# Kernel optimization log

Hardware: AMD Instinct MI355X
Metric: run time of the kernel (lower is better)

## Reference

```python
import jax, jax.numpy as jnp
import numpy as np

N = 20000   # nodes (ROIs, scaled up)
F = 20      # node_feat_dim
D = 256     # hidden_dim
H = 8       # heads
DK = D // H # 32
L = 3       # layers
S = 4       # sleep stages
E = 320000  # edges per stage


def _ln(x, g, b):
    mu = x.mean(-1, keepdims=True)
    v = ((x - mu) ** 2).mean(-1, keepdims=True)
    return (x - mu) / jnp.sqrt(v + 1e-5) * g + b


def setup_inputs() -> dict:
    key = jax.random.key(0)
    ks = jax.random.split(key, 16)
    rn = lambda k, s, sc=0.02: jax.random.normal(k, s, jnp.float32) * sc
    return {
        "x": jax.random.normal(ks[0], (N, F), jnp.float32),
        "edge_index": jax.random.randint(ks[1], (S, 2, E), 0, N, jnp.int32),
        "sc_mask": jax.random.randint(ks[2], (S, E), 0, 2, jnp.int32),
        "fc_weights": jax.random.normal(ks[3], (S, E), jnp.float32),
        "in_w": rn(ks[4], (F, D)), "in_b": jnp.zeros((D,), jnp.float32),
        "stage_emb": rn(ks[5], (S, D)),
        "Wq": rn(ks[6], (L, D, D)), "Wk": rn(ks[7], (L, D, D)),
        "Wv": rn(ks[8], (L, D, D)),
        "Wo": rn(ks[9], (L, D, D)), "bo": jnp.zeros((L, D), jnp.float32),
        "ln1_g": jnp.ones((L, D), jnp.float32), "ln1_b": jnp.zeros((L, D), jnp.float32),
        "ln2_g": jnp.ones((L, D), jnp.float32), "ln2_b": jnp.zeros((L, D), jnp.float32),
        "ffn_w1": rn(ks[10], (L, D, 4 * D)), "ffn_b1": jnp.zeros((L, 4 * D), jnp.float32),
        "ffn_w2": rn(ks[11], (L, 4 * D, D)), "ffn_b2": jnp.zeros((L, D), jnp.float32),
        "lam": jnp.full((L,), 0.5, jnp.float32),
        "fus_w": rn(ks[12], (S * D, D)), "fus_b": jnp.zeros((D,), jnp.float32),
        "out_g": jnp.ones((D,), jnp.float32), "out_b": jnp.zeros((D,), jnp.float32),
    }


def reference(x, edge_index, sc_mask, fc_weights, in_w, in_b, stage_emb,
              Wq, Wk, Wv, Wo, bo, ln1_g, ln1_b, ln2_g, ln2_b,
              ffn_w1, ffn_b1, ffn_w2, ffn_b2, lam, fus_w, fus_b, out_g, out_b):
    scale = DK ** 0.5
    stage_outs = []
    for k in range(S):  # fixed small stage count
        src, dst = edge_index[k, 0], edge_index[k, 1]
        sc = sc_mask[k].astype(jnp.float32)
        fcw = fc_weights[k]
        h = x @ in_w + in_b + stage_emb[k]
        for l in range(L):  # fixed small layer count
            Q = (h @ Wq[l]).reshape(N, H, DK)
            K = (h @ Wk[l]).reshape(N, H, DK)
            V = (h @ Wv[l]).reshape(N, H, DK)
            # edge-wise gathered dot-product scores  [E, H]
            attn = (Q[dst] * K[src]).sum(-1) / scale
            attn = attn * sc[:, None] + lam[l] * fcw[:, None]
            # segment softmax grouped by destination node (PyG softmax)
            m = jax.ops.segment_max(attn, dst, num_segments=N)
            e = jnp.exp(attn - m[dst])
            s = jax.ops.segment_sum(e, dst, num_segments=N)
            a = e / (s[dst] + 1e-16)
            # scatter-add weighted V_j  [N, H, DK]
            agg = jax.ops.segment_sum(a[:, :, None] * V[src], dst, num_segments=N)
            out = agg.reshape(N, D) @ Wo[l] + bo[l]
            out = _ln(out + h, ln1_g[l], ln1_b[l])  # residual_proj is Identity (in==out)
            f = jax.nn.gelu(out @ ffn_w1[l] + ffn_b1[l], approximate=False)
            f = f @ ffn_w2[l] + ffn_b2[l]
            h = _ln(out + f, ln2_g[l], ln2_b[l])
        stage_outs.append(h)
    h_concat = jnp.concatenate(stage_outs, axis=-1)  # [N, S*D]
    return _ln(h_concat @ fus_w + fus_b, out_g, out_b)
```

## Files before the change

kernel.cpp:

```cpp
#include <hip/hip_runtime.h>
#include <hip/hip_bf16.h>
#include <math.h>

#define N_NODES 20000
#define FDIM 20
#define DDIM 256
#define HH 8
#define LL 3
#define SS 4
#define EE 320000

typedef __attribute__((ext_vector_type(8))) short bf16x8;
typedef __attribute__((ext_vector_type(8))) unsigned short u16x8;
typedef __attribute__((ext_vector_type(4))) float f32x4;

__device__ inline unsigned short f2bf(float f) {
  unsigned u = __float_as_uint(f);
  unsigned r = u + 0x7FFFu + ((u >> 16) & 1u);
  return (unsigned short)(r >> 16);
}
__device__ inline float bf2f(unsigned short u) {
  return __uint_as_float(((unsigned)u) << 16);
}

__global__ __launch_bounds__(256) void gemm_f32_kernel(
    const float* __restrict__ A, const float* __restrict__ B,
    const float* __restrict__ bias, float* __restrict__ C,
    int M, int Nc, int K)
{
  __shared__ float As[16][65];
  __shared__ float Bs[16][65];
  const int tid = threadIdx.x;
  const int tx = tid & 15, ty = tid >> 4;
  const int row0 = blockIdx.y * 64, col0 = blockIdx.x * 64;
  const int am = tid >> 2, ak = (tid & 3) * 4;
  const int bk = tid >> 4, bc = (tid & 15) * 4;
  float acc[4][4] = {};
  for (int k0 = 0; k0 < K; k0 += 16) {
    float4 av = make_float4(0.f, 0.f, 0.f, 0.f);
    int garow = row0 + am;
    if (garow < M) {
      if (k0 + ak + 3 < K) {
        av = *(const float4*)(A + (size_t)garow * K + k0 + ak);
      } else {
        float t[4];
        #pragma unroll
        for (int j = 0; j < 4; j++)
          t[j] = (k0 + ak + j < K) ? A[(size_t)garow * K + k0 + ak + j] : 0.f;
        av = make_float4(t[0], t[1], t[2], t[3]);
      }
    }
    As[ak + 0][am] = av.x; As[ak + 1][am] = av.y;
    As[ak + 2][am] = av.z; As[ak + 3][am] = av.w;
    float4 bv = make_float4(0.f, 0.f, 0.f, 0.f);
    if (k0 + bk < K)
      bv = *(const float4*)(B + (size_t)(k0 + bk) * Nc + col0 + bc);
    Bs[bk][bc + 0] = bv.x; Bs[bk][bc + 1] = bv.y;
    Bs[bk][bc + 2] = bv.z; Bs[bk][bc + 3] = bv.w;
    __syncthreads();
    #pragma unroll
    for (int kk = 0; kk < 16; kk++) {
      float a[4], b[4];
      #pragma unroll
      for (int i = 0; i < 4; i++) a[i] = As[kk][ty * 4 + i];
      #pragma unroll
      for (int j = 0; j < 4; j++) b[j] = Bs[kk][tx * 4 + j];
      #pragma unroll
      for (int i = 0; i < 4; i++)
        #pragma unroll
        for (int j = 0; j < 4; j++)
          acc[i][j] = fmaf(a[i], b[j], acc[i][j]);
    }
    __syncthreads();
  }
  #pragma unroll
  for (int i = 0; i < 4; i++) {
    int row = row0 + ty * 4 + i;
    if (row >= M) continue;
    int col = col0 + tx * 4;
    float4 v;
    float* vp = &v.x;
    #pragma unroll
    for (int j = 0; j < 4; j++) vp[j] = acc[i][j] + bias[col + j];
    *(float4*)(C + (size_t)row * Nc + col) = v;
  }
}

template<int ACT>
__global__ __launch_bounds__(256) void mfma_gemm64(
    const unsigned short* __restrict__ A, const unsigned short* __restrict__ BT,
    const float* __restrict__ bias, unsigned short* __restrict__ Cb,
    int ldc, int M, int K, int ldb)
{
  __shared__ unsigned short As[2][64][40];
  __shared__ unsigned short Bs[2][128][40];
  const int tid = threadIdx.x, lane = tid & 63, wid = tid >> 6;
  const int wr = (wid >> 1) * 32, wc = (wid & 1) * 64;
  const int row0 = blockIdx.y * 64, col0 = blockIdx.x * 128;
  const int sr = tid >> 2, sc = (tid & 3) * 8;
  const int c15 = lane & 15, g16 = lane >> 4;
  const int KT = K >> 5;
  f32x4 acc[2][4] = {};
  int garow = row0 + sr; if (garow > M - 1) garow = M - 1;
  const unsigned short* Aptr = A + (size_t)garow * K + sc;
  const unsigned short* Bptr0 = BT + (size_t)(col0 + sr) * ldb + sc;
  const unsigned short* Bptr1 = BT + (size_t)(col0 + 64 + sr) * ldb + sc;
  u16x8 aA, b0A, b1A, aB, b0B, b1B;

#define LD64(ra, rb0, rb1, k0) { ra = *(const u16x8*)(Aptr + (k0)); \
  rb0 = *(const u16x8*)(Bptr0 + (k0)); rb1 = *(const u16x8*)(Bptr1 + (k0)); }
#define WR64(buf, ra, rb0, rb1) { *(u16x8*)&As[buf][sr][sc] = ra; \
  *(u16x8*)&Bs[buf][sr][sc] = rb0; *(u16x8*)&Bs[buf][64 + sr][sc] = rb1; }
#define MM64(buf) { bf16x8 af[2], bfv[4]; \
  _Pragma("unroll") for (int mi = 0; mi < 2; mi++) \
    af[mi] = *(const bf16x8*)&As[buf][wr + mi * 16 + c15][g16 * 8]; \
  _Pragma("unroll") for (int ni = 0; ni < 4; ni++) \
    bfv[ni] = *(const bf16x8*)&Bs[buf][wc + ni * 16 + c15][g16 * 8]; \
  _Pragma("unroll") for (int mi = 0; mi < 2; mi++) \
  _Pragma("unroll") for (int ni = 0; ni < 4; ni++) \
    acc[mi][ni] = __builtin_amdgcn_mfma_f32_16x16x32_bf16(af[mi], bfv[ni], acc[mi][ni], 0, 0, 0); }

  LD64(aA, b0A, b1A, 0);
  WR64(0, aA, b0A, b1A);
  if (KT > 1) LD64(aA, b0A, b1A, 32);
  __syncthreads();
  for (int kt = 0; kt < KT; kt += 2) {
    if (kt + 2 < KT) LD64(aB, b0B, b1B, (kt + 2) * 32);
    MM64(0);
    if (kt + 1 < KT) WR64(1, aA, b0A, b1A);
    __syncthreads();
    if (kt + 1 >= KT) break;
    if (kt + 3 < KT) LD64(aA, b0A, b1A, (kt + 3) * 32);
    MM64(1);
    if (kt + 2 < KT) WR64(0, aB, b0B, b1B);
    __syncthreads();
  }
#undef LD64
#undef WR64
#undef MM64
  #pragma unroll
  for (int mi = 0; mi < 2; mi++) {
    #pragma unroll
    for (int ni = 0; ni < 4; ni++) {
      int col = col0 + wc + ni * 16 + c15;
      float bval = bias ? bias[col] : 0.f;
      #pragma unroll
      for (int j = 0; j < 4; j++) {
        int row = row0 + wr + mi * 16 + g16 * 4 + j;
        if (row < M) {
          float t = acc[mi][ni][j] + bval;
          if (ACT == 1) t = 0.5f * t * (1.f + erff(t * 0.7071067811865475f));
          Cb[(size_t)row * ldc + col] = f2bf(t);
        }
      }
    }
  }
}

template<int KTILES, int DO_LN, int ACCUM>
__global__ __launch_bounds__(256) void gemm_ln_kernel(
    const unsigned short* __restrict__ A, const unsigned short* __restrict__ BT,
    const float* __restrict__ bias, const float* __restrict__ resid,
    const float* __restrict__ gv, const float* __restrict__ bv,
    float* __restrict__ outf, unsigned short* __restrict__ outb,
    int M, int ldb, int bk0)
{
  constexpr int K = KTILES * 32;
  __shared__ unsigned short As[2][32][40];
  __shared__ unsigned short Bs[2][256][40];
  __shared__ float red[32][4][2];
  __shared__ float stats[32][2];
  const int tid = threadIdx.x, lane = tid & 63, w = tid >> 6;
  const int row0 = blockIdx.x * 32;
  const int sr2 = tid >> 3, sc2 = (tid & 7) * 4;
  const int sr = tid >> 2, sc = (tid & 3) * 8;
  const int g16 = lane >> 4, c15 = lane & 15;
  f32x4 acc[2][4] = {};
  int garow = row0 + sr2; if (garow > M - 1) garow = M - 1;
  const unsigned short* Aptr = A + (size_t)garow * K + sc2;
  const unsigned short* Bptr0 = BT + (size_t)(0 * 64 + sr) * ldb + bk0 + sc;
  const unsigned short* Bptr1 = BT + (size_t)(1 * 64 + sr) * ldb + bk0 + sc;
  const unsigned short* Bptr2 = BT + (size_t)(2 * 64 + sr) * ldb + bk0 + sc;
  const unsigned short* Bptr3 = BT + (size_t)(3 * 64 + sr) * ldb + bk0 + sc;
  ushort4 aA, aB;
  u16x8 bA0, bA1, bA2, bA3, bB0, bB1, bB2, bB3;

#define LDGL(ra, r0, r1, r2, r3, k0) { ra = *(const ushort4*)(Aptr + (k0)); \
  r0 = *(const u16x8*)(Bptr0 + (k0)); r1 = *(const u16x8*)(Bptr1 + (k0)); \
  r2 = *(const u16x8*)(Bptr2 + (k0)); r3 = *(const u16x8*)(Bptr3 + (k0)); }
#define WRGL(buf, ra, r0, r1, r2, r3) { *(ushort4*)&As[buf][sr2][sc2] = ra; \
  *(u16x8*)&Bs[buf][0 * 64 + sr][sc] = r0; *(u16x8*)&Bs[buf][1 * 64 + sr][sc] = r1; \
  *(u16x8*)&Bs[buf][2 * 64 + sr][sc] = r2; *(u16x8*)&Bs[buf][3 * 64 + sr][sc] = r3; }
#define MMGL(buf) { bf16x8 af[2], bfv[4]; \
  _Pragma("unroll") for (int mi = 0; mi < 2; mi++) \
    af[mi] = *(const bf16x8*)&As[buf][mi * 16 + c15][g16 * 8]; \
  _Pragma("unroll") for (int ni = 0; ni < 4; ni++) \
    bfv[ni] = *(const bf16x8*)&Bs[buf][w * 64 + ni * 16 + c15][g16 * 8]; \
  _Pragma("unroll") for (int mi = 0; mi < 2; mi++) \
  _Pragma("unroll") for (int ni = 0; ni < 4; ni++) \
    acc[mi][ni] = __builtin_amdgcn_mfma_f32_16x16x32_bf16(af[mi], bfv[ni], acc[mi][ni], 0, 0, 0); }

  LDGL(aA, bA0, bA1, bA2, bA3, 0);
  WRGL(0, aA, bA0, bA1, bA2, bA3);
  if (KTILES > 1) LDGL(aA, bA0, bA1, bA2, bA3, 32);
  __syncthreads();
  for (int kt = 0; kt < KTILES; kt += 2) {
    if (kt + 2 < KTILES) LDGL(aB, bB0, bB1, bB2, bB3, (kt + 2) * 32);
    MMGL(0);
    if (kt + 1 < KTILES) WRGL(1, aA, bA0, bA1, bA2, bA3);
    __syncthreads();
    if (kt + 1 >= KTILES) break;
    if (kt + 3 < KTILES) LDGL(aA, bA0, bA1, bA2, bA3, (kt + 3) * 32);
    MMGL(1);
    if (kt + 2 < KTILES) WRGL(0, aB, bB0, bB1, bB2, bB3);
    __syncthreads();
  }
#undef LDGL
#undef WRGL
#undef MMGL
  #pragma unroll
  for (int mi = 0; mi < 2; mi++)
    #pragma unroll
    for (int ni = 0; ni < 4; ni++) {
      int col = w * 64 + ni * 16 + c15;
      float bval = bias ? bias[col] : 0.f;
      #pragma unroll
      for (int j = 0; j < 4; j++) {
        int row = row0 + mi * 16 + g16 * 4 + j;
        float t = acc[mi][ni][j] + bval;
        if (row < M) {
          if (DO_LN) t += resid[(size_t)row * DDIM + col];
          if (ACCUM) t += outf[(size_t)row * DDIM + col];
        }
        acc[mi][ni][j] = t;
      }
    }
  if (DO_LN) {
    #pragma unroll
    for (int mi = 0; mi < 2; mi++)
      #pragma unroll
      for (int j = 0; j < 4; j++) {
        float s = 0.f, q = 0.f;
        #pragma unroll
        for (int ni = 0; ni < 4; ni++) { float t = acc[mi][ni][j]; s += t; q += t * t; }
        #pragma unroll
        for (int d = 1; d < 16; d <<= 1) { s += __shfl_xor(s, d); q += __shfl_xor(q, d); }
        if (c15 == 0) {
          int r = mi * 16 + g16 * 4 + j;
          red[r][w][0] = s; red[r][w][1] = q;
        }
      }
    __syncthreads();
    if (tid < 32) {
      float s = red[tid][0][0] + red[tid][1][0] + red[tid][2][0] + red[tid][3][0];
      float q = red[tid][0][1] + red[tid][1][1] + red[tid][2][1] + red[tid][3][1];
      float mu = s * (1.f / DDIM);
      float var = q * (1.f / DDIM) - mu * mu;
      stats[tid][0] = mu;
      stats[tid][1] = rsqrtf(var + 1e-5f);
    }
    __syncthreads();
  }
  #pragma unroll
  for (int mi = 0; mi < 2; mi++)
    #pragma unroll
    for (int ni = 0; ni < 4; ni++) {
      int col = w * 64 + ni * 16 + c15;
      #pragma unroll
      for (int j = 0; j < 4; j++) {
        int r = mi * 16 + g16 * 4 + j;
        int row = row0 + r;
        if (row >= M) continue;
        float t = acc[mi][ni][j];
        float o = DO_LN ? (t - stats[r][0]) * stats[r][1] * gv[col] + bv[col] : t;
        outf[(size_t)row * DDIM + col] = o;
        if (DO_LN) outb[(size_t)row * DDIM + col] = f2bf(o);
      }
    }
}

__global__ __launch_bounds__(256) void transpose_bf16_tiled(
    const float* __restrict__ W, unsigned short* __restrict__ WT,
    int K, int Nn, int ldo, size_t istr, size_t ostr)
{
  __shared__ unsigned short t[64][65];
  const float* src = W + blockIdx.z * istr;
  unsigned short* dst = WT + blockIdx.z * ostr;
  int tid = threadIdx.x;
  int ty = tid >> 4, tx = tid & 15;
  int k0 = blockIdx.y * 64, n0 = blockIdx.x * 64;
  #pragma unroll
  for (int r = 0; r < 4; r++) {
    int k = k0 + r * 16 + ty;
    float4 v = *(const float4*)(src + (size_t)k * Nn + n0 + tx * 4);
    t[tx * 4 + 0][r * 16 + ty] = f2bf(v.x);
    t[tx * 4 + 1][r * 16 + ty] = f2bf(v.y);
    t[tx * 4 + 2][r * 16 + ty] = f2bf(v.z);
    t[tx * 4 + 3][r * 16 + ty] = f2bf(v.w);
  }
  __syncthreads();
  #pragma unroll
  for (int r = 0; r < 4; r++) {
    int n = r * 16 + ty;
    ushort4 o;
    o.x = t[n][tx * 4 + 0]; o.y = t[n][tx * 4 + 1];
    o.z = t[n][tx * 4 + 2]; o.w = t[n][tx * 4 + 3];
    *(ushort4*)(dst + (size_t)(n0 + n) * ldo + k0 + tx * 4) = o;
  }
}

__global__ void ifill_kernel(int* __restrict__ p, int v, int n) {
  int i = blockIdx.x * blockDim.x + threadIdx.x;
  if (i < n) p[i] = v;
}

__global__ void add_emb_dual(const float* __restrict__ base, const float* __restrict__ se,
                             float* __restrict__ h, unsigned short* __restrict__ hb) {
  int i4 = blockIdx.x * blockDim.x + threadIdx.x;
  if (i4 >= N_NODES * 64) return;
  float4 v = ((const float4*)base)[i4];
  float4 e = ((const float4*)se)[i4 & 63];
  v.x += e.x; v.y += e.y; v.z += e.z; v.w += e.w;
  ((float4*)h)[i4] = v;
  ushort4 o;
  o.x = f2bf(v.x); o.y = f2bf(v.y); o.z = f2bf(v.z); o.w = f2bf(v.w);
  ((ushort4*)hb)[i4] = o;
}

__global__ void hist_kernel(const int* __restrict__ dst, int* __restrict__ deg) {
  int e = blockIdx.x * blockDim.x + threadIdx.x;
  if (e < EE) atomicAdd(&deg[dst[e]], 1);
}

__global__ __launch_bounds__(1024) void scan_kernel(const int* __restrict__ deg,
                                                    int* __restrict__ rowptr) {
  __shared__ int part[1024];
  const int t = threadIdx.x;
  const int CH = (N_NODES + 1023) / 1024;
  int base = t * CH, s = 0;
  for (int i = 0; i < CH; i++) {
    int idx = base + i;
    if (idx < N_NODES) s += deg[idx];
  }
  part[t] = s;
  __syncthreads();
  for (int off = 1; off < 1024; off <<= 1) {
    int v = (t >= off) ? part[t - off] : 0;
    __syncthreads();
    part[t] += v;
    __syncthreads();
  }
  int run = (t == 0) ? 0 : part[t - 1];
  for (int i = 0; i < CH; i++) {
    int idx = base + i;
    if (idx < N_NODES) { rowptr[idx] = run; run += deg[idx]; }
  }
  if (t == 1023) rowptr[N_NODES] = run;
}

__global__ void csrfill_kernel(const int* __restrict__ src, const int* __restrict__ dst,
                               const int* __restrict__ scm, const float* __restrict__ fcw,
                               const int* __restrict__ rowptr, int* __restrict__ cur,
                               int2* __restrict__ epe) {
  int e = blockIdx.x * blockDim.x + threadIdx.x;
  if (e >= EE) return;
  int d = dst[e];
  int slot = rowptr[d] + atomicAdd(&cur[d], 1);
  epe[slot] = make_int2(src[e] | (scm[e] << 31), __float_as_int(fcw[e]));
}

__global__ __launch_bounds__(256) void attn_agg_kernel(
    const unsigned short* __restrict__ QKV,
    const int* __restrict__ rowptr, const int2* __restrict__ epe,
    const float* __restrict__ lam, int l,
    unsigned short* __restrict__ agg)
{
  int node = blockIdx.x * 4 + (threadIdx.x >> 6);
  int lane = threadIdx.x & 63;
  if (node >= N_NODES) return;
  const float laml = lam[l];
  ushort4 q4 = *(const ushort4*)(QKV + (size_t)node * 768 + lane * 4);
  float qx = bf2f(q4.x), qy = bf2f(q4.y), qz = bf2f(q4.z), qw = bf2f(q4.w);
  int beg = rowptr[node], end = rowptr[node + 1];
  float ss = 0.f;
  float a0 = 0.f, a1 = 0.f, a2 = 0.f, a3 = 0.f;
  int i = beg;
  for (; i + 3 < end; i += 4) {
    int2 e0 = epe[i], e1 = epe[i + 1], e2 = epe[i + 2], e3 = epe[i + 3];
    const unsigned short* kp0 = QKV + (size_t)(e0.x & 0x7FFFFFFF) * 768 + 256 + lane * 4;
    const unsigned short* kp1 = QKV + (size_t)(e1.x & 0x7FFFFFFF) * 768 + 256 + lane * 4;
    const unsigned short* kp2 = QKV + (size_t)(e2.x & 0x7FFFFFFF) * 768 + 256 + lane * 4;
    const unsigned short* kp3 = QKV + (size_t)(e3.x & 0x7FFFFFFF) * 768 + 256 + lane * 4;
    ushort4 k0 = *(const ushort4*)kp0, v0 = *(const ushort4*)(kp0 + 256);
    ushort4 k1 = *(const ushort4*)kp1, v1 = *(const ushort4*)(kp1 + 256);
    ushort4 k2 = *(const ushort4*)kp2, v2 = *(const ushort4*)(kp2 + 256);
    ushort4 k3 = *(const ushort4*)kp3, v3 = *(const ushort4*)(kp3 + 256);
    float d0 = qx * bf2f(k0.x) + qy * bf2f(k0.y) + qz * bf2f(k0.z) + qw * bf2f(k0.w);
    float d1 = qx * bf2f(k1.x) + qy * bf2f(k1.y) + qz * bf2f(k1.z) + qw * bf2f(k1.w);
    float d2 = qx * bf2f(k2.x) + qy * bf2f(k2.y) + qz * bf2f(k2.z) + qw * bf2f(k2.w);
    float d3 = qx * bf2f(k3.x) + qy * bf2f(k3.y) + qz * bf2f(k3.z) + qw * bf2f(k3.w);
    d0 += __shfl_xor(d0, 1); d1 += __shfl_xor(d1, 1); d2 += __shfl_xor(d2, 1); d3 += __shfl_xor(d3, 1);
    d0 += __shfl_xor(d0, 2); d1 += __shfl_xor(d1, 2); d2 += __shfl_xor(d2, 2); d3 += __shfl_xor(d3, 2);
    d0 += __shfl_xor(d0, 4); d1 += __shfl_xor(d1, 4); d2 += __shfl_xor(d2, 4); d3 += __shfl_xor(d3, 4);
    float s0 = d0 * 0.17677669529663687f * (float)(((unsigned)e0.x) >> 31) + laml * __int_as_float(e0.y);
    float s1 = d1 * 0.17677669529663687f * (float)(((unsigned)e1.x) >> 31) + laml * __int_as_float(e1.y);
    float s2 = d2 * 0.17677669529663687f * (float)(((unsigned)e2.x) >> 31) + laml * __int_as_float(e2.y);
    float s3 = d3 * 0.17677669529663687f * (float)(((unsigned)e3.x) >> 31) + laml * __int_as_float(e3.y);
    float p0 = __expf(s0), p1 = __expf(s1), p2 = __expf(s2), p3 = __expf(s3);
    ss += (p0 + p1) + (p2 + p3);
    a0 += p0 * bf2f(v0.x) + p1 * bf2f(v1.x) + p2 * bf2f(v2.x) + p3 * bf2f(v3.x);
    a1 += p0 * bf2f(v0.y) + p1 * bf2f(v1.y) + p2 * bf2f(v2.y) + p3 * bf2f(v3.y);
    a2 += p0 * bf2f(v0.z) + p1 * bf2f(v1.z) + p2 * bf2f(v2.z) + p3 * bf2f(v3.z);
    a3 += p0 * bf2f(v0.w) + p1 * bf2f(v1.w) + p2 * bf2f(v2.w) + p3 * bf2f(v3.w);
  }
  for (; i < end; i++) {
    int2 ea = epe[i];
    const unsigned short* kpa = QKV + (size_t)(ea.x & 0x7FFFFFFF) * 768 + 256 + lane * 4;
    ushort4 ka = *(const ushort4*)kpa;
    ushort4 va = *(const ushort4*)(kpa + 256);
    float da = qx * bf2f(ka.x) + qy * bf2f(ka.y) + qz * bf2f(ka.z) + qw * bf2f(ka.w);
    da += __shfl_xor(da, 1);
    da += __shfl_xor(da, 2);
    da += __shfl_xor(da, 4);
    float s0 = da * 0.17677669529663687f * (float)(((unsigned)ea.x) >> 31) + laml * __int_as_float(ea.y);
    float p0 = __expf(s0);
    ss += p0;
    a0 += p0 * bf2f(va.x);
    a1 += p0 * bf2f(va.y);
    a2 += p0 * bf2f(va.z);
    a3 += p0 * bf2f(va.w);
  }
  float inv = 1.f / (ss + 1e-16f);
  ushort4 o;
  o.x = f2bf(a0 * inv); o.y = f2bf(a1 * inv);
  o.z = f2bf(a2 * inv); o.w = f2bf(a3 * inv);
  *(ushort4*)(agg + (size_t)node * DDIM + lane * 4) = o;
}

__global__ __launch_bounds__(256) void ln_kernel(
    const float* __restrict__ X, const float* __restrict__ g,
    const float* __restrict__ b, float* __restrict__ out, int M)
{
  int row = blockIdx.x * (blockDim.x >> 6) + (threadIdx.x >> 6);
  int lane = threadIdx.x & 63;
  if (row >= M) return;
  float4 x = ((const float4*)(X + (size_t)row * DDIM))[lane];
  float s = x.x + x.y + x.z + x.w;
  #pragma unroll
  for (int mk = 1; mk < 64; mk <<= 1) s += __shfl_xor(s, mk);
  float mu = s * (1.f / DDIM);
  float d0 = x.x - mu, d1 = x.y - mu, d2 = x.z - mu, d3 = x.w - mu;
  float vs = d0 * d0 + d1 * d1 + d2 * d2 + d3 * d3;
  #pragma unroll
  for (int mk = 1; mk < 64; mk <<= 1) vs += __shfl_xor(vs, mk);
  float inv = rsqrtf(vs * (1.f / DDIM) + 1e-5f);
  float4 gg = ((const float4*)g)[lane];
  float4 bb = ((const float4*)b)[lane];
  float4 o;
  o.x = d0 * inv * gg.x + bb.x;
  o.y = d1 * inv * gg.y + bb.y;
  o.z = d2 * inv * gg.z + bb.z;
  o.w = d3 * inv * gg.w + bb.w;
  ((float4*)(out + (size_t)row * DDIM))[lane] = o;
}

extern "C" void kernel_launch(void* const* d_in, const int* in_sizes, int n_in,
                              void* d_out, int out_size, void* d_ws, size_t ws_size,
                              hipStream_t stream) {
  const float* x      = (const float*)d_in[0];
  const int*   ei     = (const int*)d_in[1];
  const int*   scm    = (const int*)d_in[2];
  const float* fcw    = (const float*)d_in[3];
  const float* in_w   = (const float*)d_in[4];
  const float* in_b   = (const float*)d_in[5];
  const float* st_emb = (const float*)d_in[6];
  const float* Wq     = (const float*)d_in[7];
  const float* Wk     = (const float*)d_in[8];
  const float* Wv     = (const float*)d_in[9];
  const float* Wo     = (const float*)d_in[10];
  const float* bo     = (const float*)d_in[11];
  const float* ln1g   = (const float*)d_in[12];
  const float* ln1b   = (const float*)d_in[13];
  const float* ln2g   = (const float*)d_in[14];
  const float* ln2b   = (const float*)d_in[15];
  const float* fw1    = (const float*)d_in[16];
  const float* fb1    = (const float*)d_in[17];
  const float* fw2    = (const float*)d_in[18];
  const float* fb2    = (const float*)d_in[19];
  const float* lam    = (const float*)d_in[20];
  const float* fus_w  = (const float*)d_in[21];
  const float* fus_b  = (const float*)d_in[22];
  const float* outg   = (const float*)d_in[23];
  const float* outb   = (const float*)d_in[24];

  const size_t ND = (size_t)N_NODES * DDIM;
  const int DD = DDIM * DDIM;
  float* W = (float*)d_ws;
  size_t off = 0;
  auto alloc = [&](size_t n) { float* p = W + off; off += n; return p; };
  float* u1 = alloc((size_t)N_NODES * 1024 / 2);
  unsigned short* f1  = (unsigned short*)u1;
  unsigned short* QKV = (unsigned short*)u1;
  unsigned short* aggb    = (unsigned short*)alloc(ND / 2);
  float* base = alloc(ND);
  float* h    = alloc(ND);
  float* out1 = alloc(ND);
  unsigned short* h_bf    = (unsigned short*)alloc(ND / 2);
  unsigned short* out1_bf = (unsigned short*)alloc(ND / 2);
  unsigned short* bfb = (unsigned short*)alloc(1310720);
  unsigned short* wqkvT = bfb;
  unsigned short* woT   = bfb + 589824;
  unsigned short* fw1T  = bfb + 786432;
  unsigned short* fw2T  = bfb + 1572864;
  unsigned short* fusT  = bfb + 2359296;
  int*  rowptr = (int*)alloc(N_NODES + 4);
  int*  deg    = (int*)alloc(N_NODES);
  int*  cur    = (int*)alloc(N_NODES);
  int2* epe    = (int2*)alloc(EE * 2);
  float* fus   = (float*)d_out;

  transpose_bf16_tiled<<<dim3(4, 4, 3), 256, 0, stream>>>(Wq, wqkvT,           DDIM, DDIM, DDIM, DD, 196608);
  transpose_bf16_tiled<<<dim3(4, 4, 3), 256, 0, stream>>>(Wk, wqkvT + 65536,   DDIM, DDIM, DDIM, DD, 196608);
  transpose_bf16_tiled<<<dim3(4, 4, 3), 256, 0, stream>>>(Wv, wqkvT + 131072,  DDIM, DDIM, DDIM, DD, 196608);
  transpose_bf16_tiled<<<dim3(4, 4, 3), 256, 0, stream>>>(Wo, woT,             DDIM, DDIM, DDIM, DD, DD);
  transpose_bf16_tiled<<<dim3(16, 4, 3), 256, 0, stream>>>(fw1, fw1T, DDIM, 4 * DDIM, DDIM, 4 * DD, 4 * DD);
  transpose_bf16_tiled<<<dim3(4, 16, 3), 256, 0, stream>>>(fw2, fw2T, 4 * DDIM, DDIM, 4 * DDIM, 4 * DD, 4 * DD);
  transpose_bf16_tiled<<<dim3(4, 16, 1), 256, 0, stream>>>(fus_w, fusT, 4 * DDIM, DDIM, 4 * DDIM, 0, 0);

  dim3 gF32(DDIM / 64, (N_NODES + 63) / 64);
  gemm_f32_kernel<<<gF32, 256, 0, stream>>>(x, in_w, in_b, base, N_NODES, DDIM, FDIM);

  const int eBlocks  = (EE + 255) / 256;
  const int n2Blocks = (2 * N_NODES + 255) / 256;
  const int lnBlocks = (N_NODES + 3) / 4;
  const int emBlocks = (N_NODES * 64 + 255) / 256;
  dim3 gQKV(6, (N_NODES + 63) / 64);
  dim3 gFFN1(8, (N_NODES + 63) / 64);
  const int fusedBlocks = (N_NODES + 31) / 32;

  for (int s = 0; s < SS; s++) {
    const int* srcp = ei + (size_t)s * 2 * EE;
    const int* dstp = srcp + EE;
    const int* scs  = scm + (size_t)s * EE;
    const float* fcs = fcw + (size_t)s * EE;

    ifill_kernel<<<n2Blocks, 256, 0, stream>>>(deg, 0, 2 * N_NODES);
    hist_kernel<<<eBlocks, 256, 0, stream>>>(dstp, deg);
    scan_kernel<<<1, 1024, 0, stream>>>(deg, rowptr);
    csrfill_kernel<<<eBlocks, 256, 0, stream>>>(srcp, dstp, scs, fcs, rowptr, cur, epe);

    add_emb_dual<<<emBlocks, 256, 0, stream>>>(base, st_emb + s * DDIM, h, h_bf);

    for (int l = 0; l < LL; l++) {
      mfma_gemm64<0><<<gQKV, 256, 0, stream>>>(
          h_bf, wqkvT + (size_t)l * 196608, nullptr, QKV, 768, N_NODES, DDIM, DDIM);

      attn_agg_kernel<<<lnBlocks, 256, 0, stream>>>(QKV, rowptr, epe, lam, l, aggb);

      gemm_ln_kernel<8, 1, 0><<<fusedBlocks, 256, 0, stream>>>(
          aggb, woT + (size_t)l * DD, bo + l * DDIM, h,
          ln1g + l * DDIM, ln1b + l * DDIM, out1, out1_bf, N_NODES, DDIM, 0);

      mfma_gemm64<1><<<gFFN1, 256, 0, stream>>>(
          out1_bf, fw1T + (size_t)l * 4 * DD, fb1 + l * 4 * DDIM, f1, 4 * DDIM,
          N_NODES, DDIM, DDIM);

      gemm_ln_kernel<32, 1, 0><<<fusedBlocks, 256, 0, stream>>>(
          f1, fw2T + (size_t)l * 4 * DD, fb2 + l * DDIM, out1,
          ln2g + l * DDIM, ln2b + l * DDIM, h, h_bf, N_NODES, 4 * DDIM, 0);
    }

    if (s == 0)
      gemm_ln_kernel<8, 0, 0><<<fusedBlocks, 256, 0, stream>>>(
          h_bf, fusT, fus_b, nullptr, nullptr, nullptr, fus, nullptr,
          N_NODES, 4 * DDIM, s * DDIM);
    else
      gemm_ln_kernel<8, 0, 1><<<fusedBlocks, 256, 0, stream>>>(
          h_bf, fusT, nullptr, nullptr, nullptr, nullptr, fus, nullptr,
          N_NODES, 4 * DDIM, s * DDIM);
  }

  ln_kernel<<<lnBlocks, 256, 0, stream>>>(fus, outg, outb, (float*)d_out, N_NODES);
}
```

Baseline: 2.827 ms.

## Enlarge MFMA GEMM tile to 128x128, pack bf16 stores, batch CSR build across stages

The QKV and FFN1 GEMMs move from 64x128 to 128x128 block tiles, with each wave computing a 64x64 subtile, to raise operand reuse per LDS load. The epilogue pairs adjacent bf16 outputs via a lane shuffle so each store writes 32 bits instead of 16. The CSR construction (histogram, scan, fill) now runs once for all four stages using blockIdx.z, replacing four serial sets of small launches. The costs are more registers and LDS per block, fewer blocks in flight, and four times the CSR buffer memory.

New measurement: 3.356 ms. 18.7% more time.

```diff
diff --git a/kernel.cpp b/kernel.cpp
--- a/kernel.cpp
+++ b/kernel.cpp
@@ -87,59 +87,60 @@
 }
 
 template<int ACT>
-__global__ __launch_bounds__(256) void mfma_gemm64(
+__global__ __launch_bounds__(256) void mfma_gemm128(
     const unsigned short* __restrict__ A, const unsigned short* __restrict__ BT,
     const float* __restrict__ bias, unsigned short* __restrict__ Cb,
     int ldc, int M, int K, int ldb)
 {
-  __shared__ unsigned short As[2][64][40];
+  __shared__ unsigned short As[2][128][40];
   __shared__ unsigned short Bs[2][128][40];
   const int tid = threadIdx.x, lane = tid & 63, wid = tid >> 6;
-  const int wr = (wid >> 1) * 32, wc = (wid & 1) * 64;
-  const int row0 = blockIdx.y * 64, col0 = blockIdx.x * 128;
-  const int sr = tid >> 2, sc = (tid & 3) * 8;
+  const int wr = (wid >> 1) * 64, wc = (wid & 1) * 64;
+  const int row0 = blockIdx.y * 128, col0 = blockIdx.x * 128;
+  const int sr = tid & 127, sc = (tid >> 7) * 16;
   const int c15 = lane & 15, g16 = lane >> 4;
   const int KT = K >> 5;
-  f32x4 acc[2][4] = {};
+  f32x4 acc[4][4] = {};
   int garow = row0 + sr; if (garow > M - 1) garow = M - 1;
   const unsigned short* Aptr = A + (size_t)garow * K + sc;
-  const unsigned short* Bptr0 = BT + (size_t)(col0 + sr) * ldb + sc;
-  const unsigned short* Bptr1 = BT + (size_t)(col0 + 64 + sr) * ldb + sc;
-  u16x8 aA, b0A, b1A, aB, b0B, b1B;
-
-#define LD64(ra, rb0, rb1, k0) { ra = *(const u16x8*)(Aptr + (k0)); \
-  rb0 = *(const u16x8*)(Bptr0 + (k0)); rb1 = *(const u16x8*)(Bptr1 + (k0)); }
-#define WR64(buf, ra, rb0, rb1) { *(u16x8*)&As[buf][sr][sc] = ra; \
-  *(u16x8*)&Bs[buf][sr][sc] = rb0; *(u16x8*)&Bs[buf][64 + sr][sc] = rb1; }
-#define MM64(buf) { bf16x8 af[2], bfv[4]; \
-  _Pragma("unroll") for (int mi = 0; mi < 2; mi++) \
+  const unsigned short* Bptr = BT + (size_t)(col0 + sr) * ldb + sc;
+  u16x8 aA0, aA1, bA0, bA1, aB0, aB1, bB0, bB1;
+
+#define LD128(a0, a1, b0, b1, k0) { \
+  a0 = *(const u16x8*)(Aptr + (k0));     a1 = *(const u16x8*)(Aptr + (k0) + 8); \
+  b0 = *(const u16x8*)(Bptr + (k0));     b1 = *(const u16x8*)(Bptr + (k0) + 8); }
+#define WR128(buf, a0, a1, b0, b1) { \
+  *(u16x8*)&As[buf][sr][sc] = a0; *(u16x8*)&As[buf][sr][sc + 8] = a1; \
+  *(u16x8*)&Bs[buf][sr][sc] = b0; *(u16x8*)&Bs[buf][sr][sc + 8] = b1; }
+#define MM128(buf) { bf16x8 af[4], bfv[4]; \
+  _Pragma("unroll") for (int mi = 0; mi < 4; mi++) \
     af[mi] = *(const bf16x8*)&As[buf][wr + mi * 16 + c15][g16 * 8]; \
   _Pragma("unroll") for (int ni = 0; ni < 4; ni++) \
     bfv[ni] = *(const bf16x8*)&Bs[buf][wc + ni * 16 + c15][g16 * 8]; \
-  _Pragma("unroll") for (int mi = 0; mi < 2; mi++) \
+  _Pragma("unroll") for (int mi = 0; mi < 4; mi++) \
   _Pragma("unroll") for (int ni = 0; ni < 4; ni++) \
     acc[mi][ni] = __builtin_amdgcn_mfma_f32_16x16x32_bf16(af[mi], bfv[ni], acc[mi][ni], 0, 0, 0); }
 
-  LD64(aA, b0A, b1A, 0);
-  WR64(0, aA, b0A, b1A);
-  if (KT > 1) LD64(aA, b0A, b1A, 32);
+  LD128(aA0, aA1, bA0, bA1, 0);
+  WR128(0, aA0, aA1, bA0, bA1);
+  if (KT > 1) LD128(aA0, aA1, bA0, bA1, 32);
   __syncthreads();
   for (int kt = 0; kt < KT; kt += 2) {
-    if (kt + 2 < KT) LD64(aB, b0B, b1B, (kt + 2) * 32);
-    MM64(0);
-    if (kt + 1 < KT) WR64(1, aA, b0A, b1A);
+    if (kt + 2 < KT) LD128(aB0, aB1, bB0, bB1, (kt + 2) * 32);
+    MM128(0);
+    if (kt + 1 < KT) WR128(1, aA0, aA1, bA0, bA1);
     __syncthreads();
     if (kt + 1 >= KT) break;
-    if (kt + 3 < KT) LD64(aA, b0A, b1A, (kt + 3) * 32);
-    MM64(1);
-    if (kt + 2 < KT) WR64(0, aB, b0B, b1B);
-    __syncthreads();
-  }
-#undef LD64
-#undef WR64
-#undef MM64
-  #pragma unroll
-  for (int mi = 0; mi < 2; mi++) {
+    if (kt + 3 < KT) LD128(aA0, aA1, bA0, bA1, (kt + 3) * 32);
+    MM128(1);
+    if (kt + 2 < KT) WR128(0, aB0, aB1, bB0, bB1);
+    __syncthreads();
+  }
+#undef LD128
+#undef WR128
+#undef MM128
+  #pragma unroll
+  for (int mi = 0; mi < 4; mi++) {
     #pragma unroll
     for (int ni = 0; ni < 4; ni++) {
       int col = col0 + wc + ni * 16 + c15;
@@ -147,11 +148,12 @@
       #pragma unroll
       for (int j = 0; j < 4; j++) {
         int row = row0 + wr + mi * 16 + g16 * 4 + j;
-        if (row < M) {
-          float t = acc[mi][ni][j] + bval;
-          if (ACT == 1) t = 0.5f * t * (1.f + erff(t * 0.7071067811865475f));
-          Cb[(size_t)row * ldc + col] = f2bf(t);
-        }
+        float t = acc[mi][ni][j] + bval;
+        if (ACT == 1) t = 0.5f * t * (1.f + erff(t * 0.7071067811865475f));
+        unsigned v = f2bf(t);
+        unsigned o = (unsigned)__shfl_xor((int)v, 1);
+        if (!(c15 & 1) && row < M)
+          *(unsigned*)(Cb + (size_t)row * ldc + col) = v | (o << 16);
       }
     }
   }
@@ -327,13 +329,19 @@
   ((ushort4*)hb)[i4] = o;
 }
 
-__global__ void hist_kernel(const int* __restrict__ dst, int* __restrict__ deg) {
+__global__ void hist_kernel(const int* __restrict__ ei, int* __restrict__ deg4) {
+  int z = blockIdx.z;
+  const int* dst = ei + (size_t)z * 2 * EE + EE;
+  int* deg = deg4 + z * N_NODES;
   int e = blockIdx.x * blockDim.x + threadIdx.x;
   if (e < EE) atomicAdd(&deg[dst[e]], 1);
 }
 
-__global__ __launch_bounds__(1024) void scan_kernel(const int* __restrict__ deg,
-                                                    int* __restrict__ rowptr) {
+__global__ __launch_bounds__(1024) void scan_kernel(const int* __restrict__ deg4,
+                                                    int* __restrict__ rowptr4) {
+  int z = blockIdx.z;
+  const int* deg = deg4 + z * N_NODES;
+  int* rowptr = rowptr4 + z * (N_NODES + 1);
   __shared__ int part[1024];
   const int t = threadIdx.x;
   const int CH = (N_NODES + 1023) / 1024;
@@ -358,15 +366,23 @@
   if (t == 1023) rowptr[N_NODES] = run;
 }
 
-__global__ void csrfill_kernel(const int* __restrict__ src, const int* __restrict__ dst,
+__global__ void csrfill_kernel(const int* __restrict__ ei,
                                const int* __restrict__ scm, const float* __restrict__ fcw,
-                               const int* __restrict__ rowptr, int* __restrict__ cur,
-                               int2* __restrict__ epe) {
+                               const int* __restrict__ rowptr4, int* __restrict__ cur4,
+                               int2* __restrict__ epe4) {
+  int z = blockIdx.z;
+  const int* src = ei + (size_t)z * 2 * EE;
+  const int* dst = src + EE;
+  const int* sc = scm + (size_t)z * EE;
+  const float* fw = fcw + (size_t)z * EE;
+  const int* rowptr = rowptr4 + z * (N_NODES + 1);
+  int* cur = cur4 + z * N_NODES;
+  int2* epe = epe4 + (size_t)z * EE;
   int e = blockIdx.x * blockDim.x + threadIdx.x;
   if (e >= EE) return;
   int d = dst[e];
   int slot = rowptr[d] + atomicAdd(&cur[d], 1);
-  epe[slot] = make_int2(src[e] | (scm[e] << 31), __float_as_int(fcw[e]));
+  epe[slot] = make_int2(src[e] | (sc[e] << 31), __float_as_int(fw[e]));
 }
 
 __global__ __launch_bounds__(256) void attn_agg_kernel(
@@ -513,10 +529,10 @@
   unsigned short* fw1T  = bfb + 786432;
   unsigned short* fw2T  = bfb + 1572864;
   unsigned short* fusT  = bfb + 2359296;
-  int*  rowptr = (int*)alloc(N_NODES + 4);
-  int*  deg    = (int*)alloc(N_NODES);
-  int*  cur    = (int*)alloc(N_NODES);
-  int2* epe    = (int2*)alloc(EE * 2);
+  int*  rowptr4 = (int*)alloc(4 * (N_NODES + 1) + 4);
+  int*  deg4    = (int*)alloc(4 * N_NODES);
+  int*  cur4    = (int*)alloc(4 * N_NODES);
+  int2* epe4    = (int2*)alloc((size_t)4 * EE * 2);
   float* fus   = (float*)d_out;
 
   transpose_bf16_tiled<<<dim3(4, 4, 3), 256, 0, stream>>>(Wq, wqkvT,           DDIM, DDIM, DDIM, DD, 196608);
@@ -527,32 +543,29 @@
   transpose_bf16_tiled<<<dim3(4, 16, 3), 256, 0, stream>>>(fw2, fw2T, 4 * DDIM, DDIM, 4 * DDIM, 4 * DD, 4 * DD);
   transpose_bf16_tiled<<<dim3(4, 16, 1), 256, 0, stream>>>(fus_w, fusT, 4 * DDIM, DDIM, 4 * DDIM, 0, 0);
 
+  const int eBlocks = (EE + 255) / 256;
+  ifill_kernel<<<(8 * N_NODES + 255) / 256, 256, 0, stream>>>(deg4, 0, 8 * N_NODES);
+  hist_kernel<<<dim3(eBlocks, 1, 4), 256, 0, stream>>>(ei, deg4);
+  scan_kernel<<<dim3(1, 1, 4), 1024, 0, stream>>>(deg4, rowptr4);
+  csrfill_kernel<<<dim3(eBlocks, 1, 4), 256, 0, stream>>>(ei, scm, fcw, rowptr4, cur4, epe4);
+
   dim3 gF32(DDIM / 64, (N_NODES + 63) / 64);
   gemm_f32_kernel<<<gF32, 256, 0, stream>>>(x, in_w, in_b, base, N_NODES, DDIM, FDIM);
 
-  const int eBlocks  = (EE + 255) / 256;
-  const int n2Blocks = (2 * N_NODES + 255) / 256;
   const int lnBlocks = (N_NODES + 3) / 4;
   const int emBlocks = (N_NODES * 64 + 255) / 256;
-  dim3 gQKV(6, (N_NODES + 63) / 64);
-  dim3 gFFN1(8, (N_NODES + 63) / 64);
+  dim3 gQKV(6, (N_NODES + 127) / 128);
+  dim3 gFFN1(8, (N_NODES + 127) / 128);
   const int fusedBlocks = (N_NODES + 31) / 32;
 
   for (int s = 0; s < SS; s++) {
-    const int* srcp = ei + (size_t)s * 2 * EE;
-    const int* dstp = srcp + EE;
-    const int* scs  = scm + (size_t)s * EE;
-    const float* fcs = fcw + (size_t)s * EE;
-
-    ifill_kernel<<<n2Blocks, 256, 0, stream>>>(deg, 0, 2 * N_NODES);
-    hist_kernel<<<eBlocks, 256, 0, stream>>>(dstp, deg);
-    scan_kernel<<<1, 1024, 0, stream>>>(deg, rowptr);
-    csrfill_kernel<<<eBlocks, 256, 0, stream>>>(srcp, dstp, scs, fcs, rowptr, cur, epe);
+    const int* rowptr = rowptr4 + s * (N_NODES + 1);
+    const int2* epe = epe4 + (size_t)s * EE;
 
     add_emb_dual<<<emBlocks, 256, 0, stream>>>(base, st_emb + s * DDIM, h, h_bf);
 
     for (int l = 0; l < LL; l++) {
-      mfma_gemm64<0><<<gQKV, 256, 0, stream>>>(
+      mfma_gemm128<0><<<gQKV, 256, 0, stream>>>(
           h_bf, wqkvT + (size_t)l * 196608, nullptr, QKV, 768, N_NODES, DDIM, DDIM);
 
       attn_agg_kernel<<<lnBlocks, 256, 0, stream>>>(QKV, rowptr, epe, lam, l, aggb);
@@ -561,7 +574,7 @@
           aggb, woT + (size_t)l * DD, bo + l * DDIM, h,
           ln1g + l * DDIM, ln1b + l * DDIM, out1, out1_bf, N_NODES, DDIM, 0);
 
-      mfma_gemm64<1><<<gFFN1, 256, 0, stream>>>(
+      mfma_gemm128<1><<<gFFN1, 256, 0, stream>>>(
           out1_bf, fw1T + (size_t)l * 4 * DD, fb1 + l * 4 * DDIM, f1, 4 * DDIM,
           N_NODES, DDIM, DDIM);
 
```
